# Performance work log

Measured on AMD Instinct MI355X. Metric: run time of the kernel, lower is better.

Reference implementation:

```python
import jax, jax.numpy as jnp
import numpy as np

N, E, B = 20000, 320000, 16
DIN, HID, HEADS, ZDIM = 128, 128, 4, 128
NEG_SLOPE = 0.2


def _glorot(key, shape):
    fan = sum(shape[-2:]) if len(shape) >= 2 else shape[-1] * 2
    return jax.random.normal(key, shape, jnp.float32) * jnp.sqrt(2.0 / fan)


def setup_inputs() -> dict:
    key = jax.random.key(0)
    ks = jax.random.split(key, 20)
    inp = {
        "x": jax.random.normal(ks[0], (N, DIN), jnp.float32),
        "edge_index": jax.random.randint(ks[1], (2, E), 0, N),
        "batch_id": jnp.sort(jax.random.randint(ks[2], (N,), 0, B)),
        "node_mask": jax.random.bernoulli(ks[3], 0.1, (N,)),
        "edge_mask": jax.random.bernoulli(ks[4], 0.5, (E,)),
    }
    # layer dims: e_Fs=[128,128,128,128]; heads=4 on layers 0,1; heads=1 last
    dims = [(DIN, HID, HEADS), (HID * HEADS, HID, HEADS), (HID * HEADS, ZDIM, 1)]
    for li, (fin, fout, h) in enumerate(dims, start=1):
        inp[f"W{li}"] = _glorot(ks[4 + 3 * li], (fin, h * fout))
        inp[f"att_src{li}"] = _glorot(ks[5 + 3 * li], (h, fout))
        inp[f"att_dst{li}"] = _glorot(ks[6 + 3 * li], (h, fout))
        inp[f"bias{li}"] = jnp.zeros((h * fout,), jnp.float32)
    return inp


def _gat_layer(x, W, a_src, a_dst, bias, src, dst, heads, fout):
    n = x.shape[0]
    h = (x @ W).reshape(n, heads, fout)            # [N,H,F]
    alpha_s = (h * a_src).sum(-1)                  # [N,H]
    alpha_d = (h * a_dst).sum(-1)                  # [N,H]
    e = jax.nn.leaky_relu(alpha_s[src] + alpha_d[dst], NEG_SLOPE)  # [E,H]
    m = jax.ops.segment_max(e, dst, num_segments=n)
    ex = jnp.exp(e - m[dst])
    denom = jax.ops.segment_sum(ex, dst, num_segments=n)
    w = ex / denom[dst]                            # segment softmax over incoming edges
    out = jax.ops.segment_sum(h[src] * w[:, :, None], dst, num_segments=n)  # [N,H,F]
    return out.reshape(n, heads * fout) + bias


def reference(x, edge_index, batch_id, node_mask, edge_mask,
              W1, att_src1, att_dst1, bias1,
              W2, att_src2, att_dst2, bias2,
              W3, att_src3, att_dst3, bias3):
    n = x.shape[0]
    loop = jnp.arange(n)
    src = jnp.concatenate([edge_index[0], loop])   # add_self_loops=True
    dst = jnp.concatenate([edge_index[1], loop])
    # edge_mask is passed as edge_attr but GATConv has edge_dim=None -> ignored
    h = _gat_layer(x, W1, att_src1, att_dst1, bias1, src, dst, HEADS, HID)
    h = jax.nn.relu(h)
    h = _gat_layer(h, W2, att_src2, att_dst2, bias2, src, dst, HEADS, HID)
    h = jax.nn.relu(h)
    h = _gat_layer(h, W3, att_src3, att_dst3, bias3, src, dst, 1, ZDIM)
    # masked global max pool: if mask.sum()>0 pool over ~mask else all nodes
    has_masked = jnp.any(node_mask)
    valid = jnp.logical_or(~node_mask, ~has_masked)
    neg = jnp.asarray(-1e30, h.dtype)
    vals = jnp.where(valid[:, None], h, neg)
    return jax.ops.segment_max(vals, batch_id, num_segments=B)
```

## Files before the change

kernel.cpp:

```cpp
#include <hip/hip_runtime.h>
#include <stdint.h>


#define NN 20000
#define MPAD 20096
#define NE 320000
#define NBATCH 16
#define NEG 0.2f
#define WSCALE 64.0f
#define WINV 0.015625f

using f16x8 = __attribute__((ext_vector_type(8))) _Float16;
using f32x4 = __attribute__((ext_vector_type(4))) float;

static __device__ __forceinline__ unsigned short h2u(_Float16 h) {
  union { _Float16 f; unsigned short u; } c;
  c.f = h;
  return c.u;
}
static __device__ __forceinline__ float f16lo(unsigned v) {
  union { unsigned short u; _Float16 f; } c;
  c.u = (unsigned short)(v & 0xFFFF);
  return (float)c.f;
}
static __device__ __forceinline__ float f16hi(unsigned v) {
  union { unsigned short u; _Float16 f; } c;
  c.u = (unsigned short)(v >> 16);
  return (float)c.f;
}
static __device__ __forceinline__ unsigned encf(float f) {
  unsigned u = __float_as_uint(f);
  return (u & 0x80000000u) ? ~u : (u | 0x80000000u);
}
static __device__ __forceinline__ float decf(unsigned u) {
  return __uint_as_float((u & 0x80000000u) ? (u ^ 0x80000000u) : ~u);
}

__global__ void k_init0(int* deg, unsigned* enc, int* flag, float* alz, int alcount) {
  int i = blockIdx.x * blockDim.x + threadIdx.x;
  if (i < NN) deg[i] = 1;
  if (i < NBATCH * 128) enc[i] = ~__float_as_uint(-1e30f);
  if (i == 0) *flag = 0;
  for (int j = i; j < alcount; j += gridDim.x * blockDim.x) alz[j] = 0.f;
}

__global__ void k_count(const int* __restrict__ ei, int* __restrict__ deg) {
  int e = blockIdx.x * blockDim.x + threadIdx.x;
  if (e < NE) atomicAdd(&deg[ei[NE + e]], 1);
}

__global__ void k_scan(const int* __restrict__ deg, int* __restrict__ row_ptr,
                       int* __restrict__ cursor) {
  __shared__ int wsum[16];
  int t = threadIdx.x;
  int lane = t & 63, wid = t >> 6;
  const int CH = 20;
  int beg = t * CH;
  int s = 0;
  for (int i = 0; i < CH; i++) {
    int idx = beg + i;
    if (idx < NN) s += deg[idx];
  }
  int incl = s;
  for (int off = 1; off < 64; off <<= 1) {
    int v = __shfl_up(incl, off, 64);
    if (lane >= off) incl += v;
  }
  if (lane == 63) wsum[wid] = incl;
  __syncthreads();
  if (t < 16) {
    int v = wsum[t];
    int in2 = v;
    for (int off = 1; off < 16; off <<= 1) {
      int u = __shfl_up(in2, off, 16);
      if (t >= off) in2 += u;
    }
    wsum[t] = in2 - v;
  }
  __syncthreads();
  int run = wsum[wid] + incl - s;
  for (int i = 0; i < CH; i++) {
    int idx = beg + i;
    if (idx < NN) {
      row_ptr[idx] = run;
      cursor[idx] = run;
      run += deg[idx];
    }
  }
  if (t == 1023) row_ptr[NN] = run;
}

__global__ void k_fill(const int* __restrict__ ei, int* __restrict__ cursor,
                       int* __restrict__ col, const int* __restrict__ nmask,
                       int* __restrict__ flag) {
  int i = blockIdx.x * blockDim.x + threadIdx.x;
  if (i >= NE + NN) return;
  int src, dst;
  if (i < NE) {
    src = ei[i];
    dst = ei[NE + i];
  } else {
    src = dst = i - NE;
    if (nmask[src] != 0) *flag = 1;
  }
  int pos = atomicAdd(&cursor[dst], 1);
  col[pos] = src;
}

#define R1 (512 * 128)
#define R2 (512 * 512)
#define R3 (128 * 512)
__global__ void k_prep(const float* __restrict__ W1, const float* __restrict__ W2,
                       const float* __restrict__ W3, const float* __restrict__ x,
                       unsigned short* __restrict__ wt1,
                       unsigned short* __restrict__ wt2,
                       unsigned short* __restrict__ wt3,
                       unsigned short* __restrict__ xp) {
  int idx = blockIdx.x * blockDim.x + threadIdx.x;
  if (idx < R1) {
    int n = idx & 511, k = idx >> 9;
    wt1[(size_t)n * 128 + k] = h2u((_Float16)(W1[(size_t)k * 512 + n] * WSCALE));
  } else if (idx < R1 + R2) {
    int j = idx - R1;
    int n = j & 511, k = j >> 9;
    wt2[(size_t)n * 512 + k] = h2u((_Float16)(W2[(size_t)k * 512 + n] * WSCALE));
  } else if (idx < R1 + R2 + R3) {
    int j = idx - (R1 + R2);
    int n = j & 127, k = j >> 7;
    wt3[(size_t)n * 512 + k] = h2u((_Float16)(W3[(size_t)k * 128 + n] * WSCALE));
  } else {
    int j = idx - (R1 + R2 + R3);
    if (j < NN * 128) xp[j] = h2u((_Float16)x[j]);
  }
}

#define BM 128
#define BN 128
#define BK 32

__global__ __launch_bounds__(256, 3) void k_gemm(
    const unsigned short* __restrict__ Ap, const unsigned short* __restrict__ Wt,
    unsigned short* __restrict__ C, const float* __restrict__ attS,
    const float* __restrict__ attD, float* __restrict__ alS,
    float* __restrict__ alD, int K, int Nc, int H) {
  __shared__ __align__(16) unsigned short As[BM][BK];
  __shared__ __align__(16) unsigned short Bs[BN][BK];
  int tid = threadIdx.x;
  int bm = blockIdx.y * BM, bn = blockIdx.x * BN;
  int wid = tid >> 6, lane = tid & 63;
  int wm = (wid >> 1) * 64, wn = (wid & 1) * 64;
  int lrow = lane & 15, lquad = lane >> 4;

  f32x4 acc[4][4] = {};

  for (int k0 = 0; k0 < K; k0 += BK) {
    __syncthreads();
#pragma unroll
    for (int i = 0; i < 2; i++) {
      int slot = tid + 256 * i;
      int row = slot >> 2;
      int ks = (slot & 3) * 8;
      *(uint4*)&As[row][ks] = *(const uint4*)(Ap + (size_t)(bm + row) * K + k0 + ks);
      *(uint4*)&Bs[row][ks] = *(const uint4*)(Wt + (size_t)(bn + row) * K + k0 + ks);
    }
    __syncthreads();

    f16x8 af[4];
#pragma unroll
    for (int mf = 0; mf < 4; mf++)
      af[mf] = *(const f16x8*)&As[wm + mf * 16 + lrow][lquad * 8];
#pragma unroll
    for (int nf = 0; nf < 4; nf++) {
      f16x8 bf = *(const f16x8*)&Bs[wn + nf * 16 + lrow][lquad * 8];
#pragma unroll
      for (int mf = 0; mf < 4; mf++)
        acc[mf][nf] =
            __builtin_amdgcn_mfma_f32_16x16x32_f16(bf, af[mf], acc[mf][nf], 0, 0, 0);
    }
  }
#pragma unroll
  for (int mf = 0; mf < 4; mf++)
#pragma unroll
    for (int nf = 0; nf < 4; nf++)
#pragma unroll
      for (int r = 0; r < 4; r++) acc[mf][nf][r] *= WINV;

  float4 aS[4], aD[4];
#pragma unroll
  for (int nf = 0; nf < 4; nf++) {
    int n0 = bn + wn + nf * 16 + lquad * 4;
    aS[nf] = *(const float4*)(attS + n0);
    aD[nf] = *(const float4*)(attD + n0);
  }
  int head = bn >> 7;
#pragma unroll
  for (int mf = 0; mf < 4; mf++) {
    float ps = 0.f, pd = 0.f;
#pragma unroll
    for (int nf = 0; nf < 4; nf++) {
      ps += acc[mf][nf][0] * aS[nf].x + acc[mf][nf][1] * aS[nf].y +
            acc[mf][nf][2] * aS[nf].z + acc[mf][nf][3] * aS[nf].w;
      pd += acc[mf][nf][0] * aD[nf].x + acc[mf][nf][1] * aD[nf].y +
            acc[mf][nf][2] * aD[nf].z + acc[mf][nf][3] * aD[nf].w;
    }
    ps += __shfl_xor(ps, 16, 64);
    ps += __shfl_xor(ps, 32, 64);
    pd += __shfl_xor(pd, 16, 64);
    pd += __shfl_xor(pd, 32, 64);
    int row = bm + wm + mf * 16 + lrow;
    if (lquad == 0) {
      atomicAdd(&alS[(size_t)row * H + head], ps);
      atomicAdd(&alD[(size_t)row * H + head], pd);
    }
  }
#pragma unroll
  for (int mf = 0; mf < 4; mf++) {
    int m = bm + wm + mf * 16 + lrow;
#pragma unroll
    for (int nf = 0; nf < 4; nf++) {
      int n0 = bn + wn + nf * 16 + lquad * 4;
      ushort4 o;
      o.x = h2u((_Float16)acc[mf][nf][0]);
      o.y = h2u((_Float16)acc[mf][nf][1]);
      o.z = h2u((_Float16)acc[mf][nf][2]);
      o.w = h2u((_Float16)acc[mf][nf][3]);
      *(ushort4*)(C + (size_t)m * Nc + n0) = o;
    }
  }
}

template <int H, int WPN, bool RELU, bool FP16OUT>
__global__ __launch_bounds__(256) void k_agg(
    const unsigned short* __restrict__ h, const float* __restrict__ as_,
    const float* __restrict__ ad_, const int* __restrict__ row_ptr,
    const int* __restrict__ col, const float* __restrict__ bias,
    float* __restrict__ out, unsigned short* __restrict__ outp) {
  constexpr int HF = H * 128, FPW = HF / WPN, PL = FPW / 64, HH = H / WPN;
  __shared__ float el[4][HH][64];
  __shared__ float wl[4][HH][64];
  __shared__ int cl[4][64];
  int tid = threadIdx.x, bwid = tid >> 6, lane = tid & 63;
  int gwid = blockIdx.x * 4 + bwid;
  int node = gwid / WPN, sub = gwid - node * WPN;
  if (node >= NN) return;
  const int hb = sub * HH;
  int beg = row_ptr[node], end = row_ptr[node + 1];
  int deg = end - beg;

  float adv[HH], m[HH], s[HH];
#pragma unroll
  for (int i = 0; i < HH; i++) {
    adv[i] = ad_[(size_t)node * H + hb + i];
    m[i] = -1e30f;
    s[i] = 0.f;
  }
  for (int j = beg + lane; j < end; j += 64) {
    int sidx = col[j];
    cl[bwid][lane] = sidx;
#pragma unroll
    for (int i = 0; i < HH; i++) {
      float e = as_[(size_t)sidx * H + hb + i] + adv[i];
      e = (e > 0.f) ? e : NEG * e;
      el[bwid][i][lane] = e;
      float nm = fmaxf(m[i], e);
      s[i] = s[i] * __expf(m[i] - nm) + __expf(e - nm);
      m[i] = nm;
    }
  }
  float Mr[HH], Sinv[HH];
#pragma unroll
  for (int i = 0; i < HH; i++) {
    float mm = m[i];
#pragma unroll
    for (int off = 32; off; off >>= 1) mm = fmaxf(mm, __shfl_xor(mm, off, 64));
    float t = s[i] * __expf(m[i] - mm);
#pragma unroll
    for (int off = 32; off; off >>= 1) t += __shfl_xor(t, off, 64);
    Mr[i] = mm;
    Sinv[i] = 1.f / t;
  }
  const int fbase = sub * FPW + lane * PL;
  const int ih = (lane * PL) >> 7;
  float acc[PL] = {};
  for (int c0 = beg; c0 < end; c0 += 64) {
    int cnt = min(64, end - c0);
    if (deg <= 64) {
      if (lane < cnt) {
#pragma unroll
        for (int i = 0; i < HH; i++)
          wl[bwid][i][lane] = __expf(el[bwid][i][lane] - Mr[i]) * Sinv[i];
      }
    } else {
      if (lane < cnt) {
        int sidx = col[c0 + lane];
        cl[bwid][lane] = sidx;
#pragma unroll
        for (int i = 0; i < HH; i++) {
          float e = as_[(size_t)sidx * H + hb + i] + adv[i];
          e = (e > 0.f) ? e : NEG * e;
          wl[bwid][i][lane] = __expf(e - Mr[i]) * Sinv[i];
        }
      }
    }
    for (int je = 0; je < cnt; je += 8) {
      float wv[8];
      int sv[8];
#pragma unroll
      for (int r = 0; r < 8; r++) {
        int ok = (je + r) < cnt;
        int idx = ok ? (je + r) : 0;
        sv[r] = cl[bwid][idx];
        wv[r] = ok ? wl[bwid][ih][idx] : 0.f;
      }
      if constexpr (PL == 4) {
        uint2 v[8];
#pragma unroll
        for (int r = 0; r < 8; r++)
          v[r] = *(const uint2*)(h + (size_t)sv[r] * HF + fbase);
#pragma unroll
        for (int r = 0; r < 8; r++) {
          acc[0] += wv[r] * f16lo(v[r].x);
          acc[1] += wv[r] * f16hi(v[r].x);
          acc[2] += wv[r] * f16lo(v[r].y);
          acc[3] += wv[r] * f16hi(v[r].y);
        }
      } else {
        unsigned v[8];
#pragma unroll
        for (int r = 0; r < 8; r++)
          v[r] = *(const unsigned*)(h + (size_t)sv[r] * HF + fbase);
#pragma unroll
        for (int r = 0; r < 8; r++) {
          acc[0] += wv[r] * f16lo(v[r]);
          acc[1] += wv[r] * f16hi(v[r]);
        }
      }
    }
  }
  float vv[PL];
#pragma unroll
  for (int i = 0; i < PL; i++) {
    float v = acc[i] + bias[fbase + i];
    if (RELU) v = fmaxf(v, 0.f);
    vv[i] = v;
  }
  if constexpr (FP16OUT) {
    if constexpr (PL == 4) {
      ushort4 o;
      o.x = h2u((_Float16)vv[0]);
      o.y = h2u((_Float16)vv[1]);
      o.z = h2u((_Float16)vv[2]);
      o.w = h2u((_Float16)vv[3]);
      *(ushort4*)(outp + (size_t)node * HF + fbase) = o;
    } else {
      ushort2 o;
      o.x = h2u((_Float16)vv[0]);
      o.y = h2u((_Float16)vv[1]);
      *(ushort2*)(outp + (size_t)node * HF + fbase) = o;
    }
  } else {
    float* op = out + (size_t)node * HF + fbase;
#pragma unroll
    for (int i = 0; i < PL; i++) op[i] = vv[i];
  }
}

__global__ void k_pool(const float* __restrict__ h, const int* __restrict__ batch,
                       const int* __restrict__ mask, const int* __restrict__ flag,
                       unsigned* __restrict__ enc) {
  int f = threadIdx.x;
  int n0 = blockIdx.x * 32;
  if (n0 >= NN) return;
  int n1 = min(NN, n0 + 32);
  int any = *flag;
  float local = -1e30f;
  int curb = batch[n0];
  for (int n = n0; n < n1; ++n) {
    int b = batch[n];
    if (b != curb) {
      if (local > -1e30f) atomicMax(&enc[curb * 128 + f], encf(local));
      local = -1e30f;
      curb = b;
    }
    bool valid = (mask[n] == 0) || (!any);
    if (valid) local = fmaxf(local, h[(size_t)n * 128 + f]);
  }
  if (local > -1e30f) atomicMax(&enc[curb * 128 + f], encf(local));
}

__global__ void k_out(const unsigned* __restrict__ enc, float* __restrict__ out) {
  int i = blockIdx.x * blockDim.x + threadIdx.x;
  if (i < NBATCH * 128) out[i] = decf(enc[i]);
}

extern "C" void kernel_launch(void* const* d_in, const int* in_sizes, int n_in,
                              void* d_out, int out_size, void* d_ws, size_t ws_size,
                              hipStream_t stream) {
  const float* x = (const float*)d_in[0];
  const int* ei = (const int*)d_in[1];
  const int* batch = (const int*)d_in[2];
  const int* nmask = (const int*)d_in[3];
  const float* W1 = (const float*)d_in[5];
  const float* as1 = (const float*)d_in[6];
  const float* ad1 = (const float*)d_in[7];
  const float* b1 = (const float*)d_in[8];
  const float* W2 = (const float*)d_in[9];
  const float* as2 = (const float*)d_in[10];
  const float* ad2 = (const float*)d_in[11];
  const float* b2 = (const float*)d_in[12];
  const float* W3 = (const float*)d_in[13];
  const float* as3 = (const float*)d_in[14];
  const float* ad3 = (const float*)d_in[15];
  const float* b3 = (const float*)d_in[16];

  char* ws = (char*)d_ws;
  size_t off = 0;
  auto alloc = [&](size_t bytes) -> char* {
    char* p = ws + off;
    off = (off + bytes + 255) & ~(size_t)255;
    return p;
  };
  unsigned short* hA = (unsigned short*)alloc((size_t)MPAD * 512 * 2);
  unsigned short* hG = (unsigned short*)alloc((size_t)MPAD * 512 * 2);
  float* out3 = (float*)alloc((size_t)MPAD * 128 * 4);
  unsigned short* xP = (unsigned short*)out3;
  unsigned short* wt1 = (unsigned short*)alloc((size_t)512 * 128 * 2);
  unsigned short* wt2 = (unsigned short*)alloc((size_t)512 * 512 * 2);
  unsigned short* wt3 = (unsigned short*)alloc((size_t)128 * 512 * 2);
  char* alStart = ws + off;
  float* alS1 = (float*)alloc((size_t)MPAD * 4 * 4);
  float* alD1 = (float*)alloc((size_t)MPAD * 4 * 4);
  float* alS2 = (float*)alloc((size_t)MPAD * 4 * 4);
  float* alD2 = (float*)alloc((size_t)MPAD * 4 * 4);
  float* alS3 = (float*)alloc((size_t)MPAD * 4);
  float* alD3 = (float*)alloc((size_t)MPAD * 4);
  int alcount = (int)(((ws + off) - alStart) / 4);
  int* deg = (int*)alloc((size_t)NN * 4);
  int* cursor = (int*)alloc((size_t)NN * 4);
  int* rowp = (int*)alloc((size_t)(NN + 1) * 4);
  int* colx = (int*)alloc((size_t)(NE + NN) * 4);
  unsigned* enc = (unsigned*)alloc((size_t)NBATCH * 128 * 4);
  int* flag = (int*)alloc(4);
  (void)ws_size; (void)n_in; (void)in_sizes; (void)out_size;

  k_init0<<<(alcount + 255) / 256, 256, 0, stream>>>((int*)deg, enc, flag,
                                                     (float*)alStart, alcount);
  k_count<<<(NE + 255) / 256, 256, 0, stream>>>(ei, deg);
  k_scan<<<1, 1024, 0, stream>>>(deg, rowp, cursor);
  k_fill<<<(NE + NN + 255) / 256, 256, 0, stream>>>(ei, cursor, colx, nmask, flag);
  {
    int total = R1 + R2 + R3 + NN * 128;
    k_prep<<<(total + 255) / 256, 256, 0, stream>>>(W1, W2, W3, x, wt1, wt2, wt3, xP);
  }

  dim3 gg1(512 / BN, MPAD / BM);
  dim3 gg3(1, MPAD / BM);

  k_gemm<<<gg1, 256, 0, stream>>>(xP, wt1, hA, as1, ad1, alS1, alD1, 128, 512, 4);
  k_agg<4, 2, true, true><<<(NN * 2 + 3) / 4, 256, 0, stream>>>(
      hA, alS1, alD1, rowp, colx, b1, nullptr, hG);
  k_gemm<<<gg1, 256, 0, stream>>>(hG, wt2, hA, as2, ad2, alS2, alD2, 512, 512, 4);
  k_agg<4, 2, true, true><<<(NN * 2 + 3) / 4, 256, 0, stream>>>(
      hA, alS2, alD2, rowp, colx, b2, nullptr, hG);
  k_gemm<<<gg3, 256, 0, stream>>>(hG, wt3, hA, as3, ad3, alS3, alD3, 512, 128, 1);
  k_agg<1, 1, false, false><<<(NN + 3) / 4, 256, 0, stream>>>(
      hA, alS3, alD3, rowp, colx, b3, out3, nullptr);

  k_pool<<<(NN + 31) / 32, 128, 0, stream>>>(out3, batch, nmask, flag, enc);
  k_out<<<(NBATCH * 128 + 255) / 256, 256, 0, stream>>>(enc, (float*)d_out);
}
```

Baseline: 356.3 us.

## Assign one wave per head in aggregation and use smaller tiles for last GEMM

Measured after the change: 359.1 us. About the same (+0.8%).

```diff
diff --git a/kernel.cpp b/kernel.cpp
--- a/kernel.cpp
+++ b/kernel.cpp
@@ -134,21 +134,22 @@
   }
 }
 
-#define BM 128
 #define BN 128
 #define BK 32
 
-__global__ __launch_bounds__(256, 3) void k_gemm(
+template <int BMT, int NT>
+__global__ __launch_bounds__(NT, 3) void k_gemm(
     const unsigned short* __restrict__ Ap, const unsigned short* __restrict__ Wt,
     unsigned short* __restrict__ C, const float* __restrict__ attS,
     const float* __restrict__ attD, float* __restrict__ alS,
     float* __restrict__ alD, int K, int Nc, int H) {
-  __shared__ __align__(16) unsigned short As[BM][BK];
+  __shared__ __align__(16) unsigned short As[BMT][BK];
   __shared__ __align__(16) unsigned short Bs[BN][BK];
   int tid = threadIdx.x;
-  int bm = blockIdx.y * BM, bn = blockIdx.x * BN;
+  int bm = blockIdx.y * BMT, bn = blockIdx.x * BN;
   int wid = tid >> 6, lane = tid & 63;
-  int wm = (wid >> 1) * 64, wn = (wid & 1) * 64;
+  int wm = (BMT == 128) ? (wid >> 1) * 64 : 0;
+  int wn = (BMT == 128) ? (wid & 1) * 64 : wid * 64;
   int lrow = lane & 15, lquad = lane >> 4;
 
   f32x4 acc[4][4] = {};
@@ -156,11 +157,17 @@
   for (int k0 = 0; k0 < K; k0 += BK) {
     __syncthreads();
 #pragma unroll
-    for (int i = 0; i < 2; i++) {
-      int slot = tid + 256 * i;
+    for (int i = 0; i < (BMT * 4) / NT; i++) {
+      int slot = tid + NT * i;
       int row = slot >> 2;
       int ks = (slot & 3) * 8;
       *(uint4*)&As[row][ks] = *(const uint4*)(Ap + (size_t)(bm + row) * K + k0 + ks);
+    }
+#pragma unroll
+    for (int i = 0; i < 512 / NT; i++) {
+      int slot = tid + NT * i;
+      int row = slot >> 2;
+      int ks = (slot & 3) * 8;
       *(uint4*)&Bs[row][ks] = *(const uint4*)(Wt + (size_t)(bn + row) * K + k0 + ks);
     }
     __syncthreads();
@@ -229,77 +236,79 @@
   }
 }
 
-template <int H, int WPN, bool RELU, bool FP16OUT>
+template <int H, bool RELU, bool FP16OUT, bool PIN>
 __global__ __launch_bounds__(256) void k_agg(
     const unsigned short* __restrict__ h, const float* __restrict__ as_,
     const float* __restrict__ ad_, const int* __restrict__ row_ptr,
     const int* __restrict__ col, const float* __restrict__ bias,
     float* __restrict__ out, unsigned short* __restrict__ outp) {
-  constexpr int HF = H * 128, FPW = HF / WPN, PL = FPW / 64, HH = H / WPN;
-  __shared__ float el[4][HH][64];
-  __shared__ float wl[4][HH][64];
+  constexpr int HF = H * 128;
+  __shared__ float wl[4][64];
   __shared__ int cl[4][64];
   int tid = threadIdx.x, bwid = tid >> 6, lane = tid & 63;
-  int gwid = blockIdx.x * 4 + bwid;
-  int node = gwid / WPN, sub = gwid - node * WPN;
-  if (node >= NN) return;
-  const int hb = sub * HH;
+  int node, sub;
+  if constexpr (PIN) {
+    sub = blockIdx.x & 3;
+    node = (blockIdx.x >> 2) * 4 + bwid;
+  } else {
+    node = blockIdx.x * 4 + bwid;
+    sub = 0;
+    if (node >= NN) return;
+  }
   int beg = row_ptr[node], end = row_ptr[node + 1];
   int deg = end - beg;
-
-  float adv[HH], m[HH], s[HH];
-#pragma unroll
-  for (int i = 0; i < HH; i++) {
-    adv[i] = ad_[(size_t)node * H + hb + i];
-    m[i] = -1e30f;
-    s[i] = 0.f;
-  }
-  for (int j = beg + lane; j < end; j += 64) {
-    int sidx = col[j];
-    cl[bwid][lane] = sidx;
-#pragma unroll
-    for (int i = 0; i < HH; i++) {
-      float e = as_[(size_t)sidx * H + hb + i] + adv[i];
+  float adv = ad_[(size_t)node * H + sub];
+  float Mr, Sinv;
+
+  if (__builtin_expect(deg <= 64, 1)) {
+    float e = -1e30f;
+    if (lane < deg) {
+      int sidx = col[beg + lane];
+      cl[bwid][lane] = sidx;
+      e = as_[(size_t)sidx * H + sub] + adv;
       e = (e > 0.f) ? e : NEG * e;
-      el[bwid][i][lane] = e;
-      float nm = fmaxf(m[i], e);
-      s[i] = s[i] * __expf(m[i] - nm) + __expf(e - nm);
-      m[i] = nm;
-    }
-  }
-  float Mr[HH], Sinv[HH];
-#pragma unroll
-  for (int i = 0; i < HH; i++) {
-    float mm = m[i];
+    }
+    float mm = e;
 #pragma unroll
     for (int off = 32; off; off >>= 1) mm = fmaxf(mm, __shfl_xor(mm, off, 64));
-    float t = s[i] * __expf(m[i] - mm);
+    float t = (lane < deg) ? __expf(e - mm) : 0.f;
+    float S = t;
+#pragma unroll
+    for (int off = 32; off; off >>= 1) S += __shfl_xor(S, off, 64);
+    Sinv = 1.f / S;
+    wl[bwid][lane] = t * Sinv;
+    Mr = mm;
+  } else {
+    float m = -1e30f, s = 0.f;
+    for (int j = beg + lane; j < end; j += 64) {
+      int sidx = col[j];
+      float e = as_[(size_t)sidx * H + sub] + adv;
+      e = (e > 0.f) ? e : NEG * e;
+      float nm = fmaxf(m, e);
+      s = s * __expf(m - nm) + __expf(e - nm);
+      m = nm;
+    }
+    float mm = m;
+#pragma unroll
+    for (int off = 32; off; off >>= 1) mm = fmaxf(mm, __shfl_xor(mm, off, 64));
+    float t = s * __expf(m - mm);
 #pragma unroll
     for (int off = 32; off; off >>= 1) t += __shfl_xor(t, off, 64);
-    Mr[i] = mm;
-    Sinv[i] = 1.f / t;
-  }
-  const int fbase = sub * FPW + lane * PL;
-  const int ih = (lane * PL) >> 7;
-  float acc[PL] = {};
+    Mr = mm;
+    Sinv = 1.f / t;
+  }
+
+  const int fbase = sub * 128 + lane * 2;
+  float acc0 = 0.f, acc1 = 0.f;
   for (int c0 = beg; c0 < end; c0 += 64) {
     int cnt = min(64, end - c0);
-    if (deg <= 64) {
-      if (lane < cnt) {
-#pragma unroll
-        for (int i = 0; i < HH; i++)
-          wl[bwid][i][lane] = __expf(el[bwid][i][lane] - Mr[i]) * Sinv[i];
-      }
-    } else {
+    if (deg > 64) {
       if (lane < cnt) {
         int sidx = col[c0 + lane];
         cl[bwid][lane] = sidx;
-#pragma unroll
-        for (int i = 0; i < HH; i++) {
-          float e = as_[(size_t)sidx * H + hb + i] + adv[i];
-          e = (e > 0.f) ? e : NEG * e;
-          wl[bwid][i][lane] = __expf(e - Mr[i]) * Sinv[i];
-        }
+        float e = as_[(size_t)sidx * H + sub] + adv;
+        e = (e > 0.f) ? e : NEG * e;
+        wl[bwid][lane] = __expf(e - Mr) * Sinv;
       }
     }
     for (int je = 0; je < cnt; je += 8) {
@@ -310,58 +319,32 @@
         int ok = (je + r) < cnt;
         int idx = ok ? (je + r) : 0;
         sv[r] = cl[bwid][idx];
-        wv[r] = ok ? wl[bwid][ih][idx] : 0.f;
+        wv[r] = ok ? wl[bwid][idx] : 0.f;
       }
-      if constexpr (PL == 4) {
-        uint2 v[8];
-#pragma unroll
-        for (int r = 0; r < 8; r++)
-          v[r] = *(const uint2*)(h + (size_t)sv[r] * HF + fbase);
-#pragma unroll
-        for (int r = 0; r < 8; r++) {
-          acc[0] += wv[r] * f16lo(v[r].x);
-          acc[1] += wv[r] * f16hi(v[r].x);
-          acc[2] += wv[r] * f16lo(v[r].y);
-          acc[3] += wv[r] * f16hi(v[r].y);
-        }
-      } else {
-        unsigned v[8];
-#pragma unroll
-        for (int r = 0; r < 8; r++)
-          v[r] = *(const unsigned*)(h + (size_t)sv[r] * HF + fbase);
-#pragma unroll
-        for (int r = 0; r < 8; r++) {
-          acc[0] += wv[r] * f16lo(v[r]);
-          acc[1] += wv[r] * f16hi(v[r]);
-        }
+      unsigned v[8];
+#pragma unroll
+      for (int r = 0; r < 8; r++)
+        v[r] = *(const unsigned*)(h + (size_t)sv[r] * HF + fbase);
+#pragma unroll
+      for (int r = 0; r < 8; r++) {
+        acc0 += wv[r] * f16lo(v[r]);
+        acc1 += wv[r] * f16hi(v[r]);
       }
     }
   }
-  float vv[PL];
-#pragma unroll
-  for (int i = 0; i < PL; i++) {
-    float v = acc[i] + bias[fbase + i];
-    if (RELU) v = fmaxf(v, 0.f);
-    vv[i] = v;
+  float v0 = acc0 + bias[fbase], v1 = acc1 + bias[fbase + 1];
+  if (RELU) {
+    v0 = fmaxf(v0, 0.f);
+    v1 = fmaxf(v1, 0.f);
   }
   if constexpr (FP16OUT) {
-    if constexpr (PL == 4) {
-      ushort4 o;
-      o.x = h2u((_Float16)vv[0]);
-      o.y = h2u((_Float16)vv[1]);
-      o.z = h2u((_Float16)vv[2]);
-      o.w = h2u((_Float16)vv[3]);
-      *(ushort4*)(outp + (size_t)node * HF + fbase) = o;
-    } else {
-      ushort2 o;
-      o.x = h2u((_Float16)vv[0]);
-      o.y = h2u((_Float16)vv[1]);
-      *(ushort2*)(outp + (size_t)node * HF + fbase) = o;
-    }
+    ushort2 o;
+    o.x = h2u((_Float16)v0);
+    o.y = h2u((_Float16)v1);
+    *(ushort2*)(outp + (size_t)node * HF + fbase) = o;
   } else {
-    float* op = out + (size_t)node * HF + fbase;
-#pragma unroll
-    for (int i = 0; i < PL; i++) op[i] = vv[i];
+    float2 o = make_float2(v0, v1);
+    *(float2*)(out + (size_t)node * HF + fbase) = o;
   }
 }
 
@@ -453,17 +436,20 @@
     k_prep<<<(total + 255) / 256, 256, 0, stream>>>(W1, W2, W3, x, wt1, wt2, wt3, xP);
   }
 
-  dim3 gg1(512 / BN, MPAD / BM);
-  dim3 gg3(1, MPAD / BM);
-
-  k_gemm<<<gg1, 256, 0, stream>>>(xP, wt1, hA, as1, ad1, alS1, alD1, 128, 512, 4);
-  k_agg<4, 2, true, true><<<(NN * 2 + 3) / 4, 256, 0, stream>>>(
-      hA, alS1, alD1, rowp, colx, b1, nullptr, hG);
-  k_gemm<<<gg1, 256, 0, stream>>>(hG, wt2, hA, as2, ad2, alS2, alD2, 512, 512, 4);
-  k_agg<4, 2, true, true><<<(NN * 2 + 3) / 4, 256, 0, stream>>>(
-      hA, alS2, alD2, rowp, colx, b2, nullptr, hG);
-  k_gemm<<<gg3, 256, 0, stream>>>(hG, wt3, hA, as3, ad3, alS3, alD3, 512, 128, 1);
-  k_agg<1, 1, false, false><<<(NN + 3) / 4, 256, 0, stream>>>(
+  dim3 gg1(512 / BN, MPAD / 128);
+  dim3 gg3(1, MPAD / 64);
+
+  k_gemm<128, 256><<<gg1, 256, 0, stream>>>(xP, wt1, hA, as1, ad1, alS1, alD1,
+                                            128, 512, 4);
+  k_agg<4, true, true, true><<<NN, 256, 0, stream>>>(hA, alS1, alD1, rowp, colx,
+                                                     b1, nullptr, hG);
+  k_gemm<128, 256><<<gg1, 256, 0, stream>>>(hG, wt2, hA, as2, ad2, alS2, alD2,
+                                            512, 512, 4);
+  k_agg<4, true, true, true><<<NN, 256, 0, stream>>>(hA, alS2, alD2, rowp, colx,
+                                                     b2, nullptr, hG);
+  k_gemm<64, 128><<<gg3, 128, 0, stream>>>(hG, wt3, hA, as3, ad3, alS3, alD3,
+                                           512, 128, 1);
+  k_agg<1, false, false, false><<<(NN + 3) / 4, 256, 0, stream>>>(
       hA, alS3, alD3, rowp, colx, b3, out3, nullptr);
 
   k_pool<<<(NN + 31) / 32, 128, 0, stream>>>(out3, batch, nmask, flag, enc);
```
